# Kernel optimization log

Hardware: AMD Instinct MI355X
Metric: run time of the kernel (lower is better)

The kernel has to match this reference:

```python
import jax, jax.numpy as jnp
import numpy as np
from jax import lax

T, B, D = 2048, 16, 1024

def _xavier(key, shape):
    limit = np.sqrt(6.0 / (shape[0] + shape[1])).astype(np.float32)
    return jax.random.uniform(key, shape, jnp.float32, -limit, limit)

def setup_inputs() -> dict:
    key = jax.random.key(0)
    kx, ka, kk, kv = jax.random.split(key, 4)
    return {
        "x": jax.random.normal(kx, (T, B, D), jnp.float32),
        "h0": jnp.zeros((B, D), jnp.float32),
        "W_alpha": _xavier(ka, (D, D)),
        "b_alpha": jnp.full((D,), 2.0, jnp.float32),
        "W_k": _xavier(kk, (D, D)),
        "b_k": jnp.full((D,), -2.0, jnp.float32),
        "W_v": _xavier(kv, (D, D)),
        "b_v": jnp.zeros((D,), jnp.float32),
    }

def reference(x, h0, W_alpha, b_alpha, W_k, b_k, W_v, b_v):
    # Gate projections: x @ W.T + b, batched over (T, B). Shapes: [T,B,D]
    alpha = jax.nn.sigmoid(jnp.einsum('tbd,ed->tbe', x, W_alpha) + b_alpha)
    k = jax.nn.sigmoid(jnp.einsum('tbd,ed->tbe', x, W_k) + b_k)
    v = jnp.tanh(jnp.einsum('tbd,ed->tbe', x, W_v) + b_v)
    retain = alpha * (1.0 - k)   # a_t
    write = k * v                # b_t
    # Diagonal linear recurrence h_t = a_t * h_{t-1} + b_t via scan
    def step(h, ab):
        a, b = ab
        h_new = a * h + b
        return h_new, h_new
    _, hs = lax.scan(step, h0, (retain, write))  # hs: [T,B,D]
    h = jnp.concatenate([h0[None], hs], axis=0)  # [T+1,B,D], includes h0
    # output_t = h_t * silu(h_t) = h_t^2 * sigmoid(h_t)
    output = hs * hs * jax.nn.sigmoid(hs)
    return (output, h)
```

## Files before the change

### kernel.cpp

```cpp
#include <hip/hip_runtime.h>
#include <cstdint>

#define T_DIM 2048
#define B_DIM 16
#define D_DIM 1024
#define M_DIM (T_DIM * B_DIM)
#define BD (B_DIM * D_DIM)
#define BD4 (BD / 4)
#define CCH 64
#define LCH (T_DIM / CCH)

typedef _Float16 f16x8 __attribute__((ext_vector_type(8)));
typedef float f32x4 __attribute__((ext_vector_type(4)));

__device__ __forceinline__ void async_cp16(const void* g, void* l) {
  __builtin_amdgcn_global_load_lds(
      (const __attribute__((address_space(1))) void*)(uintptr_t)g,
      (__attribute__((address_space(3))) void*)(uint32_t)(uintptr_t)l,
      16, 0, 0);
}

__device__ __forceinline__ float sigmoidf_(float z) {
  return 1.f / (1.f + __expf(-z));
}
__device__ __forceinline__ float tanhf_(float z) {
  float t = __expf(2.f * z);
  return (t - 1.f) / (t + 1.f);
}

__global__ void cvt_f32_f16(const float* __restrict__ s, _Float16* __restrict__ d, int n8) {
  int i = blockIdx.x * blockDim.x + threadIdx.x;
  if (i >= n8) return;
  const float4* sp = (const float4*)s;
  float4 u = sp[2 * i];
  float4 v = sp[2 * i + 1];
  f16x8 o;
  o[0] = (_Float16)u.x; o[1] = (_Float16)u.y; o[2] = (_Float16)u.z; o[3] = (_Float16)u.w;
  o[4] = (_Float16)v.x; o[5] = (_Float16)v.y; o[6] = (_Float16)v.z; o[7] = (_Float16)v.w;
  *(f16x8*)(d + (size_t)i * 8) = o;
}

__global__ __launch_bounds__(512, 2) void gate_gemm(
    const _Float16* __restrict__ x16,
    const _Float16* __restrict__ wa16,
    const _Float16* __restrict__ wk16,
    const _Float16* __restrict__ wv16,
    const float* __restrict__ ba, const float* __restrict__ bk, const float* __restrict__ bv,
    float* __restrict__ Aret, float* __restrict__ Bwr) {
  __shared__ __align__(16) char smem[98304];

  const int tid  = threadIdx.x;
  const int wid  = tid >> 6;
  const int lane = tid & 63;
  const int wm = wid >> 2;
  const int wn = wid & 3;
  const int lr = lane & 15;
  const int kg = lane >> 4;

  const int m0 = blockIdx.x * 128;
  const int n0 = blockIdx.y * 128;

  const int arow = tid >> 2;
  const int achk = tid & 3;
  const int aswz = achk ^ ((arow >> 1) & 3);

  f32x4 acc[3][4][2];
#pragma unroll
  for (int w = 0; w < 3; ++w)
#pragma unroll
    for (int mi = 0; mi < 4; ++mi)
#pragma unroll
      for (int ni = 0; ni < 2; ++ni)
        acc[w][mi][ni] = (f32x4)0.f;

  const size_t gA0 = (size_t)(m0 + arow) * D_DIM + aswz * 8;
  const size_t gB0 = (size_t)(n0 + arow) * D_DIM + aswz * 8;

  auto stage = [&](int buf, int kk) {
    char* base = smem + buf * 32768;
    async_cp16(x16  + gA0 + kk * 32, base         + tid * 16);
    async_cp16(wa16 + gB0 + kk * 32, base +  8192 + tid * 16);
    async_cp16(wk16 + gB0 + kk * 32, base + 16384 + tid * 16);
    async_cp16(wv16 + gB0 + kk * 32, base + 24576 + tid * 16);
  };

  const int slot = (kg ^ ((lr >> 1) & 3)) * 8;

  auto compute = [&](int buf) {
    const _Float16* bufA = (const _Float16*)(smem + buf * 32768);
    const _Float16* bufB = bufA + 4096;
    f16x8 af[4];
#pragma unroll
    for (int mi = 0; mi < 4; ++mi)
      af[mi] = *(const f16x8*)&bufA[(wm * 64 + mi * 16 + lr) * 32 + slot];
#pragma unroll
    for (int w = 0; w < 3; ++w) {
      f16x8 b0 = *(const f16x8*)&bufB[(w * 128 + wn * 32 + lr) * 32 + slot];
      f16x8 b1 = *(const f16x8*)&bufB[(w * 128 + wn * 32 + 16 + lr) * 32 + slot];
#pragma unroll
      for (int mi = 0; mi < 4; ++mi) {
        acc[w][mi][0] = __builtin_amdgcn_mfma_f32_16x16x32_f16(af[mi], b0, acc[w][mi][0], 0, 0, 0);
        acc[w][mi][1] = __builtin_amdgcn_mfma_f32_16x16x32_f16(af[mi], b1, acc[w][mi][1], 0, 0, 0);
      }
    }
  };

  stage(0, 0);
  stage(1, 1);
#pragma unroll 1
  for (int kk = 0; kk < 30; ++kk) {
    stage((kk + 2) % 3, kk + 2);
    asm volatile("s_waitcnt vmcnt(8)" ::: "memory");
    __builtin_amdgcn_s_barrier();
    compute(kk % 3);
    asm volatile("s_waitcnt lgkmcnt(0)" ::: "memory");
    __builtin_amdgcn_s_barrier();
  }
  asm volatile("s_waitcnt vmcnt(4)" ::: "memory");
  __builtin_amdgcn_s_barrier();
  compute(0);
  asm volatile("s_waitcnt lgkmcnt(0)" ::: "memory");
  __builtin_amdgcn_s_barrier();
  asm volatile("s_waitcnt vmcnt(0)" ::: "memory");
  __builtin_amdgcn_s_barrier();
  compute(1);
  asm volatile("s_waitcnt lgkmcnt(0)" ::: "memory");
  __builtin_amdgcn_s_barrier();

  float* tb = (float*)smem + wid * (32 * 33);
  const float ba_[2] = { ba[n0 + wn * 32 + lr], ba[n0 + wn * 32 + 16 + lr] };
  const float bk_[2] = { bk[n0 + wn * 32 + lr], bk[n0 + wn * 32 + 16 + lr] };
  const float bv_[2] = { bv[n0 + wn * 32 + lr], bv[n0 + wn * 32 + 16 + lr] };

#pragma unroll
  for (int arr = 0; arr < 2; ++arr) {
    float* dst = arr ? Bwr : Aret;
#pragma unroll
    for (int half = 0; half < 2; ++half) {
#pragma unroll
      for (int ni = 0; ni < 2; ++ni)
#pragma unroll
        for (int m2 = 0; m2 < 2; ++m2) {
          const int mi = half * 2 + m2;
#pragma unroll
          for (int r = 0; r < 4; ++r) {
            float za = acc[0][mi][ni][r] + ba_[ni];
            float zk = acc[1][mi][ni][r] + bk_[ni];
            float val;
            if (arr == 0) {
              val = sigmoidf_(za) * (1.f - sigmoidf_(zk));
            } else {
              float zv = acc[2][mi][ni][r] + bv_[ni];
              val = sigmoidf_(zk) * tanhf_(zv);
            }
            tb[(m2 * 16 + kg * 4 + r) * 33 + ni * 16 + lr] = val;
          }
        }
      __syncthreads();
#pragma unroll
      for (int i = 0; i < 4; ++i) {
        const int rl = i * 8 + (lane >> 3);
        const int cc = (lane & 7) * 4;
        float4 v;
        v.x = tb[rl * 33 + cc + 0];
        v.y = tb[rl * 33 + cc + 1];
        v.z = tb[rl * 33 + cc + 2];
        v.w = tb[rl * 33 + cc + 3];
        const size_t m = (size_t)(m0 + wm * 64 + half * 32 + rl);
        *(float4*)&dst[m * D_DIM + n0 + wn * 32 + cc] = v;
      }
      __syncthreads();
    }
  }
}

__device__ __forceinline__ float4 f4fma(float4 a, float4 h, float4 b) {
  float4 r;
  r.x = fmaf(a.x, h.x, b.x); r.y = fmaf(a.y, h.y, b.y);
  r.z = fmaf(a.z, h.z, b.z); r.w = fmaf(a.w, h.w, b.w);
  return r;
}
__device__ __forceinline__ float4 f4mul(float4 a, float4 b) {
  float4 r; r.x = a.x*b.x; r.y = a.y*b.y; r.z = a.z*b.z; r.w = a.w*b.w; return r;
}

__global__ void scan_phase1(const float4* __restrict__ A4, const float4* __restrict__ B4,
                            float4* __restrict__ cP, float4* __restrict__ cS) {
  int tid = blockIdx.x * 256 + threadIdx.x;
  int bd4 = tid & (BD4 - 1);
  int c   = tid >> 12;
  size_t base = (size_t)c * LCH * BD4 + bd4;
  float4 P = make_float4(1.f, 1.f, 1.f, 1.f);
  float4 S = make_float4(0.f, 0.f, 0.f, 0.f);
#pragma unroll 4
  for (int t = 0; t < LCH; ++t) {
    float4 a = A4[base + (size_t)t * BD4];
    float4 b = B4[base + (size_t)t * BD4];
    S = f4fma(a, S, b);
    P = f4mul(P, a);
  }
  cP[tid] = P;
  cS[tid] = S;
}

__global__ void scan_phase2(const float4* __restrict__ h0q,
                            const float4* __restrict__ cP, const float4* __restrict__ cS,
                            float4* __restrict__ hst, float4* __restrict__ houtq) {
  int bd4 = blockIdx.x * 64 + threadIdx.x;
  float4 h = h0q[bd4];
  houtq[bd4] = h;
#pragma unroll 4
  for (int c = 0; c < CCH; ++c) {
    hst[(size_t)c * BD4 + bd4] = h;
    h = f4fma(cP[(size_t)c * BD4 + bd4], h, cS[(size_t)c * BD4 + bd4]);
  }
}

__global__ void scan_phase3(const float4* __restrict__ hst,
                            float4* __restrict__ Aq, float4* __restrict__ Bq) {
  int tid = blockIdx.x * 256 + threadIdx.x;
  int bd4 = tid & (BD4 - 1);
  int c   = tid >> 12;
  size_t base = (size_t)c * LCH * BD4 + bd4;
  float4 h = hst[(size_t)c * BD4 + bd4];
#pragma unroll 4
  for (int t = 0; t < LCH; ++t) {
    size_t off = base + (size_t)t * BD4;
    float4 a = Aq[off];
    float4 b = Bq[off];
    h = f4fma(a, h, b);
    Bq[off] = h;
    float4 o;
    o.x = h.x * h.x * sigmoidf_(h.x);
    o.y = h.y * h.y * sigmoidf_(h.y);
    o.z = h.z * h.z * sigmoidf_(h.z);
    o.w = h.w * h.w * sigmoidf_(h.w);
    Aq[off] = o;
  }
}

extern "C" void kernel_launch(void* const* d_in, const int* in_sizes, int n_in,
                              void* d_out, int out_size, void* d_ws, size_t ws_size,
                              hipStream_t stream) {
  const float* x  = (const float*)d_in[0];
  const float* h0 = (const float*)d_in[1];
  const float* Wa = (const float*)d_in[2];
  const float* ba = (const float*)d_in[3];
  const float* Wk = (const float*)d_in[4];
  const float* bk = (const float*)d_in[5];
  const float* Wv = (const float*)d_in[6];
  const float* bv = (const float*)d_in[7];

  float* out  = (float*)d_out;
  float* hout = out + (size_t)M_DIM * D_DIM;

  float* Aret = out;
  float* Bwr  = hout + BD;

  char* ws = (char*)d_ws;
  _Float16* x16  = (_Float16*)ws;
  _Float16* wa16 = (_Float16*)(ws + 67108864);
  _Float16* wk16 = (_Float16*)(ws + 67108864 + 2097152);
  _Float16* wv16 = (_Float16*)(ws + 67108864 + 2 * 2097152);
  float4* cP  = (float4*)ws;
  float4* cS  = cP + (size_t)CCH * BD4;
  float4* hst = cS + (size_t)CCH * BD4;

  const int nx8 = M_DIM * D_DIM / 8;
  const int nw8 = D_DIM * D_DIM / 8;
  cvt_f32_f16<<<dim3((nx8 + 255) / 256), dim3(256), 0, stream>>>(x, x16, nx8);
  cvt_f32_f16<<<dim3((nw8 + 255) / 256), dim3(256), 0, stream>>>(Wa, wa16, nw8);
  cvt_f32_f16<<<dim3((nw8 + 255) / 256), dim3(256), 0, stream>>>(Wk, wk16, nw8);
  cvt_f32_f16<<<dim3((nw8 + 255) / 256), dim3(256), 0, stream>>>(Wv, wv16, nw8);

  gate_gemm<<<dim3(M_DIM / 128, D_DIM / 128), dim3(512), 0, stream>>>(
      x16, wa16, wk16, wv16, ba, bk, bv, Aret, Bwr);

  scan_phase1<<<dim3(CCH * BD4 / 256), dim3(256), 0, stream>>>(
      (const float4*)Aret, (const float4*)Bwr, cP, cS);
  scan_phase2<<<dim3(BD4 / 64), dim3(64), 0, stream>>>(
      (const float4*)h0, cP, cS, hst, (float4*)hout);
  scan_phase3<<<dim3(CCH * BD4 / 256), dim3(256), 0, stream>>>(
      hst, (float4*)Aret, (float4*)Bwr);
}
```

Baseline: 764.6 us.

## Pack retain/write gates as fp16 pairs in one buffer and reorder GEMM tiles

The gate GEMM now writes retain and write as one packed fp16x2 word per element into a single buffer instead of two separate fp32 arrays. This halves the bytes written by the GEMM and read by both scan passes. Block indexing is linearized so consecutive blocks share the same M rows across N tiles, and the k-loop is unrolled by three with s_setprio around the MFMA compute. Storing the gates in fp16 reduces precision of the recurrence coefficients, and the error can accumulate over the scan.

```diff
diff --git a/kernel.cpp b/kernel.cpp
--- a/kernel.cpp
+++ b/kernel.cpp
@@ -11,6 +11,7 @@
 #define LCH (T_DIM / CCH)
 
 typedef _Float16 f16x8 __attribute__((ext_vector_type(8)));
+typedef _Float16 f16x2 __attribute__((ext_vector_type(2)));
 typedef float f32x4 __attribute__((ext_vector_type(4)));
 
 __device__ __forceinline__ void async_cp16(const void* g, void* l) {
@@ -26,6 +27,15 @@
 __device__ __forceinline__ float tanhf_(float z) {
   float t = __expf(2.f * z);
   return (t - 1.f) / (t + 1.f);
+}
+
+__device__ __forceinline__ uint32_t pack2(float a, float b) {
+  f16x2 h; h[0] = (_Float16)a; h[1] = (_Float16)b;
+  uint32_t u; __builtin_memcpy(&u, &h, 4); return u;
+}
+__device__ __forceinline__ float2 unpack2(uint32_t u) {
+  f16x2 h; __builtin_memcpy(&h, &u, 4);
+  return make_float2((float)h[0], (float)h[1]);
 }
 
 __global__ void cvt_f32_f16(const float* __restrict__ s, _Float16* __restrict__ d, int n8) {
@@ -46,7 +56,7 @@
     const _Float16* __restrict__ wk16,
     const _Float16* __restrict__ wv16,
     const float* __restrict__ ba, const float* __restrict__ bk, const float* __restrict__ bv,
-    float* __restrict__ Aret, float* __restrict__ Bwr) {
+    uint32_t* __restrict__ AB) {
   __shared__ __align__(16) char smem[98304];
 
   const int tid  = threadIdx.x;
@@ -57,8 +67,9 @@
   const int lr = lane & 15;
   const int kg = lane >> 4;
 
-  const int m0 = blockIdx.x * 128;
-  const int n0 = blockIdx.y * 128;
+  const int lin = blockIdx.x;
+  const int m0 = (lin >> 3) * 128;
+  const int n0 = (lin & 7) * 128;
 
   const int arow = tid >> 2;
   const int achk = tid & 3;
@@ -105,16 +116,24 @@
     }
   };
 
+#define STEP(CB, SB, KNEXT)                                   \
+  stage(SB, KNEXT);                                           \
+  asm volatile("s_waitcnt vmcnt(8)" ::: "memory");            \
+  __builtin_amdgcn_s_barrier();                               \
+  __builtin_amdgcn_s_setprio(1);                              \
+  compute(CB);                                                \
+  __builtin_amdgcn_s_setprio(0);                              \
+  asm volatile("s_waitcnt lgkmcnt(0)" ::: "memory");          \
+  __builtin_amdgcn_s_barrier();                               \
+  __builtin_amdgcn_sched_barrier(0);
+
   stage(0, 0);
   stage(1, 1);
 #pragma unroll 1
-  for (int kk = 0; kk < 30; ++kk) {
-    stage((kk + 2) % 3, kk + 2);
-    asm volatile("s_waitcnt vmcnt(8)" ::: "memory");
-    __builtin_amdgcn_s_barrier();
-    compute(kk % 3);
-    asm volatile("s_waitcnt lgkmcnt(0)" ::: "memory");
-    __builtin_amdgcn_s_barrier();
+  for (int kk = 0; kk < 30; kk += 3) {
+    STEP(0, 2, kk + 2)
+    STEP(1, 0, kk + 3)
+    STEP(2, 1, kk + 4)
   }
   asm volatile("s_waitcnt vmcnt(4)" ::: "memory");
   __builtin_amdgcn_s_barrier();
@@ -126,65 +145,48 @@
   compute(1);
   asm volatile("s_waitcnt lgkmcnt(0)" ::: "memory");
   __builtin_amdgcn_s_barrier();
-
-  float* tb = (float*)smem + wid * (32 * 33);
+  __builtin_amdgcn_sched_barrier(0);
+#undef STEP
+
+  uint32_t* tbu = (uint32_t*)smem + wid * (32 * 33);
   const float ba_[2] = { ba[n0 + wn * 32 + lr], ba[n0 + wn * 32 + 16 + lr] };
   const float bk_[2] = { bk[n0 + wn * 32 + lr], bk[n0 + wn * 32 + 16 + lr] };
   const float bv_[2] = { bv[n0 + wn * 32 + lr], bv[n0 + wn * 32 + 16 + lr] };
 
 #pragma unroll
-  for (int arr = 0; arr < 2; ++arr) {
-    float* dst = arr ? Bwr : Aret;
-#pragma unroll
-    for (int half = 0; half < 2; ++half) {
-#pragma unroll
-      for (int ni = 0; ni < 2; ++ni)
-#pragma unroll
-        for (int m2 = 0; m2 < 2; ++m2) {
-          const int mi = half * 2 + m2;
-#pragma unroll
-          for (int r = 0; r < 4; ++r) {
-            float za = acc[0][mi][ni][r] + ba_[ni];
-            float zk = acc[1][mi][ni][r] + bk_[ni];
-            float val;
-            if (arr == 0) {
-              val = sigmoidf_(za) * (1.f - sigmoidf_(zk));
-            } else {
-              float zv = acc[2][mi][ni][r] + bv_[ni];
-              val = sigmoidf_(zk) * tanhf_(zv);
-            }
-            tb[(m2 * 16 + kg * 4 + r) * 33 + ni * 16 + lr] = val;
-          }
+  for (int half = 0; half < 2; ++half) {
+#pragma unroll
+    for (int ni = 0; ni < 2; ++ni)
+#pragma unroll
+      for (int m2 = 0; m2 < 2; ++m2) {
+        const int mi = half * 2 + m2;
+#pragma unroll
+        for (int r = 0; r < 4; ++r) {
+          float sa = sigmoidf_(acc[0][mi][ni][r] + ba_[ni]);
+          float sk = sigmoidf_(acc[1][mi][ni][r] + bk_[ni]);
+          float tv = tanhf_(acc[2][mi][ni][r] + bv_[ni]);
+          tbu[(m2 * 16 + kg * 4 + r) * 33 + ni * 16 + lr] =
+              pack2(sa * (1.f - sk), sk * tv);
         }
-      __syncthreads();
-#pragma unroll
-      for (int i = 0; i < 4; ++i) {
-        const int rl = i * 8 + (lane >> 3);
-        const int cc = (lane & 7) * 4;
-        float4 v;
-        v.x = tb[rl * 33 + cc + 0];
-        v.y = tb[rl * 33 + cc + 1];
-        v.z = tb[rl * 33 + cc + 2];
-        v.w = tb[rl * 33 + cc + 3];
-        const size_t m = (size_t)(m0 + wm * 64 + half * 32 + rl);
-        *(float4*)&dst[m * D_DIM + n0 + wn * 32 + cc] = v;
       }
-      __syncthreads();
+    __syncthreads();
+#pragma unroll
+    for (int i = 0; i < 4; ++i) {
+      const int rl = i * 8 + (lane >> 3);
+      const int cc = (lane & 7) * 4;
+      uint4 v;
+      v.x = tbu[rl * 33 + cc + 0];
+      v.y = tbu[rl * 33 + cc + 1];
+      v.z = tbu[rl * 33 + cc + 2];
+      v.w = tbu[rl * 33 + cc + 3];
+      const size_t m = (size_t)(m0 + wm * 64 + half * 32 + rl);
+      *(uint4*)&AB[m * D_DIM + n0 + wn * 32 + cc] = v;
     }
-  }
-}
-
-__device__ __forceinline__ float4 f4fma(float4 a, float4 h, float4 b) {
-  float4 r;
-  r.x = fmaf(a.x, h.x, b.x); r.y = fmaf(a.y, h.y, b.y);
-  r.z = fmaf(a.z, h.z, b.z); r.w = fmaf(a.w, h.w, b.w);
-  return r;
-}
-__device__ __forceinline__ float4 f4mul(float4 a, float4 b) {
-  float4 r; r.x = a.x*b.x; r.y = a.y*b.y; r.z = a.z*b.z; r.w = a.w*b.w; return r;
-}
-
-__global__ void scan_phase1(const float4* __restrict__ A4, const float4* __restrict__ B4,
+    __syncthreads();
+  }
+}
+
+__global__ void scan_phase1(const uint4* __restrict__ AB,
                             float4* __restrict__ cP, float4* __restrict__ cS) {
   int tid = blockIdx.x * 256 + threadIdx.x;
   int bd4 = tid & (BD4 - 1);
@@ -194,10 +196,12 @@
   float4 S = make_float4(0.f, 0.f, 0.f, 0.f);
 #pragma unroll 4
   for (int t = 0; t < LCH; ++t) {
-    float4 a = A4[base + (size_t)t * BD4];
-    float4 b = B4[base + (size_t)t * BD4];
-    S = f4fma(a, S, b);
-    P = f4mul(P, a);
+    uint4 u = AB[base + (size_t)t * BD4];
+    float2 e0 = unpack2(u.x), e1 = unpack2(u.y), e2 = unpack2(u.z), e3 = unpack2(u.w);
+    S.x = fmaf(e0.x, S.x, e0.y); P.x *= e0.x;
+    S.y = fmaf(e1.x, S.y, e1.y); P.y *= e1.x;
+    S.z = fmaf(e2.x, S.z, e2.y); P.z *= e2.x;
+    S.w = fmaf(e3.x, S.w, e3.y); P.w *= e3.x;
   }
   cP[tid] = P;
   cS[tid] = S;
@@ -212,12 +216,14 @@
 #pragma unroll 4
   for (int c = 0; c < CCH; ++c) {
     hst[(size_t)c * BD4 + bd4] = h;
-    h = f4fma(cP[(size_t)c * BD4 + bd4], h, cS[(size_t)c * BD4 + bd4]);
+    float4 p = cP[(size_t)c * BD4 + bd4], s = cS[(size_t)c * BD4 + bd4];
+    h.x = fmaf(p.x, h.x, s.x); h.y = fmaf(p.y, h.y, s.y);
+    h.z = fmaf(p.z, h.z, s.z); h.w = fmaf(p.w, h.w, s.w);
   }
 }
 
 __global__ void scan_phase3(const float4* __restrict__ hst,
-                            float4* __restrict__ Aq, float4* __restrict__ Bq) {
+                            float4* __restrict__ outq, uint4* ABq) {
   int tid = blockIdx.x * 256 + threadIdx.x;
   int bd4 = tid & (BD4 - 1);
   int c   = tid >> 12;
@@ -226,16 +232,19 @@
 #pragma unroll 4
   for (int t = 0; t < LCH; ++t) {
     size_t off = base + (size_t)t * BD4;
-    float4 a = Aq[off];
-    float4 b = Bq[off];
-    h = f4fma(a, h, b);
-    Bq[off] = h;
+    uint4 u = ABq[off];
+    float2 e0 = unpack2(u.x), e1 = unpack2(u.y), e2 = unpack2(u.z), e3 = unpack2(u.w);
+    h.x = fmaf(e0.x, h.x, e0.y);
+    h.y = fmaf(e1.x, h.y, e1.y);
+    h.z = fmaf(e2.x, h.z, e2.y);
+    h.w = fmaf(e3.x, h.w, e3.y);
+    *(float4*)&ABq[off] = h;
     float4 o;
     o.x = h.x * h.x * sigmoidf_(h.x);
     o.y = h.y * h.y * sigmoidf_(h.y);
     o.z = h.z * h.z * sigmoidf_(h.z);
     o.w = h.w * h.w * sigmoidf_(h.w);
-    Aq[off] = o;
+    outq[off] = o;
   }
 }
 
@@ -254,8 +263,7 @@
   float* out  = (float*)d_out;
   float* hout = out + (size_t)M_DIM * D_DIM;
 
-  float* Aret = out;
-  float* Bwr  = hout + BD;
+  uint32_t* AB = (uint32_t*)(hout + BD);
 
   char* ws = (char*)d_ws;
   _Float16* x16  = (_Float16*)ws;
@@ -273,13 +281,13 @@
   cvt_f32_f16<<<dim3((nw8 + 255) / 256), dim3(256), 0, stream>>>(Wk, wk16, nw8);
   cvt_f32_f16<<<dim3((nw8 + 255) / 256), dim3(256), 0, stream>>>(Wv, wv16, nw8);
 
-  gate_gemm<<<dim3(M_DIM / 128, D_DIM / 128), dim3(512), 0, stream>>>(
-      x16, wa16, wk16, wv16, ba, bk, bv, Aret, Bwr);
+  gate_gemm<<<dim3(2048), dim3(512), 0, stream>>>(
+      x16, wa16, wk16, wv16, ba, bk, bv, AB);
 
   scan_phase1<<<dim3(CCH * BD4 / 256), dim3(256), 0, stream>>>(
-      (const float4*)Aret, (const float4*)Bwr, cP, cS);
+      (const uint4*)AB, cP, cS);
   scan_phase2<<<dim3(BD4 / 64), dim3(64), 0, stream>>>(
       (const float4*)h0, cP, cS, hst, (float4*)hout);
   scan_phase3<<<dim3(CCH * BD4 / 256), dim3(256), 0, stream>>>(
-      hst, (float4*)Aret, (float4*)Bwr);
-}
+      hst, (float4*)out, (uint4*)AB);
+}
```

Result: faster. 700.8 us (-8.3%).
